# Optimization experiments

Hardware: AMD Instinct MI355X
Metric: run time of the kernel (lower is better)

## Reference

```python
import jax, jax.numpy as jnp
import numpy as np

FP8_MAX = 448.0  # torch.finfo(float8_e4m3fn).max


def per_tensor_quantize(t):
    amax = jnp.max(jnp.abs(t))
    scale = jnp.maximum(amax, 1e-12) / FP8_MAX
    q = jnp.clip(t / scale, -FP8_MAX, FP8_MAX)
    return q, scale.astype(jnp.float32)


def fp8_cast(t):
    # round-to-fp8-e4m3 and back (value-faithful to .to(float8_e4m3fn)),
    # straight-through so it is also usable under vjp
    rounded = t.astype(jnp.float8_e4m3fn).astype(t.dtype)
    return t + jax.lax.stop_gradient(rounded - t)


def setup_inputs() -> dict:
    key = jax.random.key(0)
    k1, k2, k3 = jax.random.split(key, 3)
    B, S, D_IN, D_OUT = 4, 2048, 4096, 4096
    x = jax.random.normal(k1, (B, S, D_IN), dtype=jnp.float32)
    # build a pre-quantized weight exactly like the repo would: quantize a float weight
    w = jax.random.normal(k2, (D_OUT, D_IN), dtype=jnp.float32) * 0.02
    qweight, weight_scale = per_tensor_quantize(w)
    bias = jax.random.normal(k3, (D_OUT,), dtype=jnp.float32) * 0.01
    return {"x": x, "qweight": qweight, "weight_scale": weight_scale, "bias": bias}


def reference(x, qweight, weight_scale, bias):
    quantize_output = True  # init kwarg
    # quantize activation per-tensor
    qinput, input_scale = per_tensor_quantize(x)
    qinput = fp8_cast(qinput)          # .to(float8_e4m3fn)
    qw = fp8_cast(qweight)             # .to(qdtype)
    # dequant-scaled GEMM: linear(A*sa, B*sb) + bias
    a = qinput * input_scale.astype(x.dtype)
    b = qw * weight_scale.astype(x.dtype)
    out = jnp.einsum('bsd,od->bso', a, b) + bias
    if quantize_output:
        qout, out_scale = per_tensor_quantize(out)  # clamp only, no fp8 cast (matches torch)
        out = qout * out_scale
    return out
```

## Files before the change

kernel.cpp:

```cpp
#include <hip/hip_runtime.h>
#include <stdint.h>

#define FP8_MAX 448.0f

typedef float f32x16 __attribute__((ext_vector_type(16)));
typedef int i32x8 __attribute__((ext_vector_type(8)));


__device__ __forceinline__ void async_load16(const void* gptr, void* lptr) {
  __builtin_amdgcn_global_load_lds(
      (const __attribute__((address_space(1))) unsigned int*)(uintptr_t)gptr,
      (__attribute__((address_space(3))) unsigned int*)(unsigned)(uintptr_t)lptr,
      16, 0, 0);
}

__device__ __forceinline__ unsigned pack4_fp8(float a, float b, float c, float d) {
  int v = __builtin_amdgcn_cvt_pk_fp8_f32(a, b, 0, false);
  v = __builtin_amdgcn_cvt_pk_fp8_f32(c, d, v, true);
  return (unsigned)v;
}

__device__ __forceinline__ float clip_fp8(float q) {
  return fminf(FP8_MAX, fmaxf(-FP8_MAX, q));
}

__device__ __forceinline__ i32x8 frag32(const unsigned char* rowbase, int o_lo) {
  uint4 lo = *(const uint4*)(rowbase + o_lo);
  uint4 hi = *(const uint4*)(rowbase + (o_lo ^ 16));
  i32x8 f;
  f[0] = lo.x; f[1] = lo.y; f[2] = lo.z; f[3] = lo.w;
  f[4] = hi.x; f[5] = hi.y; f[6] = hi.z; f[7] = hi.w;
  return f;
}


__global__ void k_amax(const float4* __restrict__ x, long n4, unsigned* __restrict__ out) {
  float m = 0.f;
  const long stride = (long)gridDim.x * blockDim.x;
  for (long i = (long)blockIdx.x * blockDim.x + threadIdx.x; i < n4; i += stride) {
    float4 v = x[i];
    m = fmaxf(m, fmaxf(fmaxf(fabsf(v.x), fabsf(v.y)), fmaxf(fabsf(v.z), fabsf(v.w))));
  }
#pragma unroll
  for (int off = 32; off > 0; off >>= 1)
    m = fmaxf(m, __shfl_xor(m, off, 64));
  __shared__ float sm[4];
  const int wv = threadIdx.x >> 6;
  if ((threadIdx.x & 63) == 0) sm[wv] = m;
  __syncthreads();
  if (threadIdx.x == 0) {
    m = fmaxf(fmaxf(sm[0], sm[1]), fmaxf(sm[2], sm[3]));
    atomicMax(out, __float_as_uint(m));
  }
}


__global__ void k_quant_x(const float4* __restrict__ x, unsigned* __restrict__ q,
                          const unsigned* __restrict__ amax_bits) {
  const float scale = fmaxf(__uint_as_float(*amax_bits), 1e-12f) / 448.0f;
  const long i0 = (long)blockIdx.x * blockDim.x + threadIdx.x;
  const long stride = (long)gridDim.x * blockDim.x;
#pragma unroll
  for (int r = 0; r < 4; r++) {
    const long i = i0 + r * stride;
    float4 v = x[i];
    q[i] = pack4_fp8(clip_fp8(v.x / scale), clip_fp8(v.y / scale),
                     clip_fp8(v.z / scale), clip_fp8(v.w / scale));
  }
}


__global__ void k_quant_w(const float4* __restrict__ w, unsigned* __restrict__ q) {
  const long i0 = (long)blockIdx.x * blockDim.x + threadIdx.x;
  const long stride = (long)gridDim.x * blockDim.x;
#pragma unroll
  for (int r = 0; r < 4; r++) {
    const long i = i0 + r * stride;
    float4 v = w[i];
    q[i] = pack4_fp8(clip_fp8(v.x), clip_fp8(v.y), clip_fp8(v.z), clip_fp8(v.w));
  }
}


__global__ __launch_bounds__(512, 2) void k_gemm(
    const unsigned char* __restrict__ qa, const unsigned char* __restrict__ qb,
    const unsigned* __restrict__ amax_bits, const float* __restrict__ wscale,
    const float* __restrict__ bias, float* __restrict__ out,
    int M, int N, int K) {
  __shared__ unsigned char lds[98304];

  const int t = threadIdx.x;
  const int lane = t & 63;
  const int wv = t >> 6;
  const int wm = wv >> 2;
  const int wn = wv & 3;
  const int lr = lane & 31;
  const int h = lane >> 5;
  const int key = (lr >> 1) & 3;

  const int bx = blockIdx.x;
  const int by = blockIdx.y;

  const unsigned char* Ag = qa + (size_t)by * 256 * K;
  const unsigned char* Bg = qb + (size_t)bx * 256 * K;

  size_t g_off[2]; int l_off[2];
#pragma unroll
  for (int r = 0; r < 2; r++) {
    const int idx = t + r * 512;
    const int row = idx >> 2;
    const int cs = idx & 3;
    g_off[r] = (size_t)row * K + (size_t)((cs ^ ((row >> 1) & 3)) << 4);
    l_off[r] = idx << 4;
  }

  const int o_lo = ((2 * h) ^ key) << 4;
  const int a_rowoff = (wm * 128 + lr) * 64;
  const int b_rowoff = (wn * 64 + lr) * 64;

  f32x16 acc[4][2];
#pragma unroll
  for (int i = 0; i < 4; i++)
#pragma unroll
    for (int j = 0; j < 2; j++)
#pragma unroll
      for (int r = 0; r < 16; r++) acc[i][j][r] = 0.f;

  int a0 = 0, a1 = 16384, a2 = 32768;
  int b0 = 49152, b1 = 65536, b2 = 81920;

#pragma unroll
  for (int r = 0; r < 2; r++) {
    async_load16(Ag + g_off[r], lds + a0 + l_off[r]);
    async_load16(Bg + g_off[r], lds + b0 + l_off[r]);
  }
#pragma unroll
  for (int r = 0; r < 2; r++) {
    async_load16(Ag + g_off[r] + 64, lds + a1 + l_off[r]);
    async_load16(Bg + g_off[r] + 64, lds + b1 + l_off[r]);
  }
  asm volatile("s_waitcnt vmcnt(4)" ::: "memory");
  __builtin_amdgcn_s_barrier();
  asm volatile("" ::: "memory");

  const int NT = K >> 6;
  for (int tile = 0; tile < NT; ++tile) {
    const bool haveS = (tile + 2 < NT);
    const size_t kb2 = (size_t)(tile + 2) << 6;
    const unsigned char* pa = lds + a0 + a_rowoff;
    const unsigned char* pb = lds + b0 + b_rowoff;

    i32x8 af0 = frag32(pa, o_lo);
    i32x8 af1 = frag32(pa + 2048, o_lo);
    i32x8 bf0 = frag32(pb, o_lo);
    i32x8 bf1 = frag32(pb + 2048, o_lo);
    if (haveS) {
#pragma unroll
      for (int r = 0; r < 2; r++)
        async_load16(Ag + g_off[r] + kb2, lds + a2 + l_off[r]);
#pragma unroll
      for (int r = 0; r < 2; r++)
        async_load16(Bg + g_off[r] + kb2, lds + b2 + l_off[r]);
    }
    i32x8 af2 = frag32(pa + 4096, o_lo);
    i32x8 af3 = frag32(pa + 6144, o_lo);

    __builtin_amdgcn_s_setprio(1);
    acc[0][0] = __builtin_amdgcn_mfma_scale_f32_32x32x64_f8f6f4(
        af0, bf0, acc[0][0], 0, 0, 0, 0x7f7f7f7f, 0, 0x7f7f7f7f);
    acc[0][1] = __builtin_amdgcn_mfma_scale_f32_32x32x64_f8f6f4(
        af0, bf1, acc[0][1], 0, 0, 0, 0x7f7f7f7f, 0, 0x7f7f7f7f);
    acc[1][0] = __builtin_amdgcn_mfma_scale_f32_32x32x64_f8f6f4(
        af1, bf0, acc[1][0], 0, 0, 0, 0x7f7f7f7f, 0, 0x7f7f7f7f);
    acc[1][1] = __builtin_amdgcn_mfma_scale_f32_32x32x64_f8f6f4(
        af1, bf1, acc[1][1], 0, 0, 0, 0x7f7f7f7f, 0, 0x7f7f7f7f);
    acc[2][0] = __builtin_amdgcn_mfma_scale_f32_32x32x64_f8f6f4(
        af2, bf0, acc[2][0], 0, 0, 0, 0x7f7f7f7f, 0, 0x7f7f7f7f);
    acc[2][1] = __builtin_amdgcn_mfma_scale_f32_32x32x64_f8f6f4(
        af2, bf1, acc[2][1], 0, 0, 0, 0x7f7f7f7f, 0, 0x7f7f7f7f);
    acc[3][0] = __builtin_amdgcn_mfma_scale_f32_32x32x64_f8f6f4(
        af3, bf0, acc[3][0], 0, 0, 0, 0x7f7f7f7f, 0, 0x7f7f7f7f);
    acc[3][1] = __builtin_amdgcn_mfma_scale_f32_32x32x64_f8f6f4(
        af3, bf1, acc[3][1], 0, 0, 0, 0x7f7f7f7f, 0, 0x7f7f7f7f);
    __builtin_amdgcn_s_setprio(0);

    if (haveS) {
      asm volatile("s_waitcnt vmcnt(4)" ::: "memory");
    } else {
      asm volatile("s_waitcnt vmcnt(0)" ::: "memory");
    }
    __builtin_amdgcn_s_barrier();
    asm volatile("" ::: "memory");

    int ta = a0; a0 = a1; a1 = a2; a2 = ta;
    int tb = b0; b0 = b1; b1 = b2; b2 = tb;
  }

  const float s_comb =
      (fmaxf(__uint_as_float(*amax_bits), 1e-12f) / 448.0f) * wscale[0];
#pragma unroll
  for (int nj = 0; nj < 2; ++nj) {
    const int col = bx * 256 + wn * 64 + nj * 32 + lr;
    const float bv = bias[col];
#pragma unroll
    for (int mi = 0; mi < 4; ++mi) {
      const int row0 = by * 256 + wm * 128 + mi * 32 + 4 * h;
#pragma unroll
      for (int r = 0; r < 16; ++r) {
        const int row = row0 + (r & 3) + 8 * (r >> 2);
        out[(size_t)row * N + col] = acc[mi][nj][r] * s_comb + bv;
      }
    }
  }
}


extern "C" void kernel_launch(void* const* d_in, const int* in_sizes, int n_in,
                              void* d_out, int out_size, void* d_ws, size_t ws_size,
                              hipStream_t stream) {
  const float* x = (const float*)d_in[0];
  const float* qw = (const float*)d_in[1];
  const float* wscale = (const float*)d_in[2];
  const float* bias = (const float*)d_in[3];

  const int N = in_sizes[3];
  const int K = in_sizes[1] / N;
  const int M = in_sizes[0] / K;

  const long nx = (long)M * K;
  const long nw = (long)N * K;

  unsigned char* ws = (unsigned char*)d_ws;
  unsigned* amax_bits = (unsigned*)ws;
  unsigned char* qx8 = ws + 256;
  unsigned char* qw8 = qx8 + nx;

  float* out = (float*)d_out;

  hipMemsetAsync(d_ws, 0, 4, stream);
  k_amax<<<2048, 256, 0, stream>>>((const float4*)x, nx / 4, amax_bits);
  k_quant_x<<<(int)(nx / 4 / 4 / 256), 256, 0, stream>>>(
      (const float4*)x, (unsigned*)qx8, amax_bits);
  k_quant_w<<<(int)(nw / 4 / 4 / 256), 256, 0, stream>>>(
      (const float4*)qw, (unsigned*)qw8);
  dim3 grid(N / 256, M / 256);
  k_gemm<<<grid, 512, 0, stream>>>(qx8, qw8, amax_bits, wscale, bias, out,
                                   M, N, K);
}
```

Measured before the change: 452.6 us.

## Software-pipeline LDS fragment loads with MFMAs via register double-buffering

The GEMM main loop is unrolled by two and now keeps two sets of B-fragment registers. The next tile's fragments are read from LDS while the current tile's second half of MFMAs is still issuing, instead of being read before any MFMA starts. The barrier and the global-to-LDS prefetch move to the middle of the tile body, and the wait becomes vmcnt(0). The intent is to hide LDS read latency behind matrix-core work, at the cost of more live registers and an unroll that assumes an even tile count.

```diff
diff --git a/kernel.cpp b/kernel.cpp
--- a/kernel.cpp
+++ b/kernel.cpp
@@ -82,6 +82,47 @@
 }
 
 
+#define MFMA_F8(d, a, b)                                                     \
+  d = __builtin_amdgcn_mfma_scale_f32_32x32x64_f8f6f4(a, b, d, 0, 0, 0,      \
+                                                      0x7f7f7f7f, 0, 0x7f7f7f7f)
+
+#define GEMM_BODY(T, bc0, bc1, bn0, bn1)                                     \
+  {                                                                          \
+    const bool hv1 = ((T) + 1 < NT);                                         \
+    const bool hv2 = ((T) + 2 < NT);                                         \
+    __builtin_amdgcn_s_setprio(1);                                           \
+    MFMA_F8(acc[0][0], af0, bc0); MFMA_F8(acc[0][1], af0, bc1);              \
+    MFMA_F8(acc[1][0], af1, bc0); MFMA_F8(acc[1][1], af1, bc1);              \
+    __builtin_amdgcn_s_setprio(0);                                           \
+    __builtin_amdgcn_sched_barrier(0);                                       \
+    if (hv1) {                                                               \
+      asm volatile("s_waitcnt vmcnt(0)" ::: "memory");                       \
+      __builtin_amdgcn_s_barrier();                                          \
+      const unsigned char* pa = lds + rA + a_rowoff;                         \
+      const unsigned char* pb = lds + rB + b_rowoff;                         \
+      af0 = frag32(pa, o_lo);                                                \
+      af1 = frag32(pa + 2048, o_lo);                                         \
+      bn0 = frag32(pb, o_lo);                                                \
+      bn1 = frag32(pb + 2048, o_lo);                                         \
+      if (hv2) {                                                             \
+        const size_t kb = (size_t)((T) + 2) << 6;                            \
+        async_load16(Ag + g_off[0] + kb, lds + sA + l_off[0]);               \
+        async_load16(Ag + g_off[1] + kb, lds + sA + l_off[1]);               \
+        async_load16(Bg + g_off[0] + kb, lds + sB + l_off[0]);               \
+        async_load16(Bg + g_off[1] + kb, lds + sB + l_off[1]);               \
+      }                                                                      \
+    }                                                                        \
+    __builtin_amdgcn_sched_barrier(0);                                       \
+    __builtin_amdgcn_s_setprio(1);                                           \
+    MFMA_F8(acc[2][0], af2, bc0); MFMA_F8(acc[2][1], af2, bc1);              \
+    if (hv1) af2 = frag32(lds + rA + a_rowoff + 4096, o_lo);                 \
+    MFMA_F8(acc[3][0], af3, bc0); MFMA_F8(acc[3][1], af3, bc1);              \
+    if (hv1) af3 = frag32(lds + rA + a_rowoff + 6144, o_lo);                 \
+    __builtin_amdgcn_s_setprio(0);                                           \
+    { int tmp = fA; fA = rA; rA = sA; sA = tmp; }                            \
+    { int tmp = fB; fB = rB; rB = sB; sB = tmp; }                            \
+  }
+
 __global__ __launch_bounds__(512, 2) void k_gemm(
     const unsigned char* __restrict__ qa, const unsigned char* __restrict__ qb,
     const unsigned* __restrict__ amax_bits, const float* __restrict__ wscale,
@@ -126,74 +167,38 @@
 #pragma unroll
       for (int r = 0; r < 16; r++) acc[i][j][r] = 0.f;
 
-  int a0 = 0, a1 = 16384, a2 = 32768;
-  int b0 = 49152, b1 = 65536, b2 = 81920;
+  int fA = 0, rA = 16384, sA = 32768;
+  int fB = 49152, rB = 65536, sB = 81920;
 
 #pragma unroll
   for (int r = 0; r < 2; r++) {
-    async_load16(Ag + g_off[r], lds + a0 + l_off[r]);
-    async_load16(Bg + g_off[r], lds + b0 + l_off[r]);
+    async_load16(Ag + g_off[r], lds + fA + l_off[r]);
+    async_load16(Bg + g_off[r], lds + fB + l_off[r]);
   }
 #pragma unroll
   for (int r = 0; r < 2; r++) {
-    async_load16(Ag + g_off[r] + 64, lds + a1 + l_off[r]);
-    async_load16(Bg + g_off[r] + 64, lds + b1 + l_off[r]);
+    async_load16(Ag + g_off[r] + 64, lds + rA + l_off[r]);
+    async_load16(Bg + g_off[r] + 64, lds + rB + l_off[r]);
   }
   asm volatile("s_waitcnt vmcnt(4)" ::: "memory");
   __builtin_amdgcn_s_barrier();
-  asm volatile("" ::: "memory");
+
+  i32x8 af0, af1, af2, af3, bfA0, bfA1, bfB0, bfB1;
+  {
+    const unsigned char* pa = lds + fA + a_rowoff;
+    const unsigned char* pb = lds + fB + b_rowoff;
+    af0 = frag32(pa, o_lo);
+    af1 = frag32(pa + 2048, o_lo);
+    af2 = frag32(pa + 4096, o_lo);
+    af3 = frag32(pa + 6144, o_lo);
+    bfA0 = frag32(pb, o_lo);
+    bfA1 = frag32(pb + 2048, o_lo);
+  }
 
   const int NT = K >> 6;
-  for (int tile = 0; tile < NT; ++tile) {
-    const bool haveS = (tile + 2 < NT);
-    const size_t kb2 = (size_t)(tile + 2) << 6;
-    const unsigned char* pa = lds + a0 + a_rowoff;
-    const unsigned char* pb = lds + b0 + b_rowoff;
-
-    i32x8 af0 = frag32(pa, o_lo);
-    i32x8 af1 = frag32(pa + 2048, o_lo);
-    i32x8 bf0 = frag32(pb, o_lo);
-    i32x8 bf1 = frag32(pb + 2048, o_lo);
-    if (haveS) {
-#pragma unroll
-      for (int r = 0; r < 2; r++)
-        async_load16(Ag + g_off[r] + kb2, lds + a2 + l_off[r]);
-#pragma unroll
-      for (int r = 0; r < 2; r++)
-        async_load16(Bg + g_off[r] + kb2, lds + b2 + l_off[r]);
-    }
-    i32x8 af2 = frag32(pa + 4096, o_lo);
-    i32x8 af3 = frag32(pa + 6144, o_lo);
-
-    __builtin_amdgcn_s_setprio(1);
-    acc[0][0] = __builtin_amdgcn_mfma_scale_f32_32x32x64_f8f6f4(
-        af0, bf0, acc[0][0], 0, 0, 0, 0x7f7f7f7f, 0, 0x7f7f7f7f);
-    acc[0][1] = __builtin_amdgcn_mfma_scale_f32_32x32x64_f8f6f4(
-        af0, bf1, acc[0][1], 0, 0, 0, 0x7f7f7f7f, 0, 0x7f7f7f7f);
-    acc[1][0] = __builtin_amdgcn_mfma_scale_f32_32x32x64_f8f6f4(
-        af1, bf0, acc[1][0], 0, 0, 0, 0x7f7f7f7f, 0, 0x7f7f7f7f);
-    acc[1][1] = __builtin_amdgcn_mfma_scale_f32_32x32x64_f8f6f4(
-        af1, bf1, acc[1][1], 0, 0, 0, 0x7f7f7f7f, 0, 0x7f7f7f7f);
-    acc[2][0] = __builtin_amdgcn_mfma_scale_f32_32x32x64_f8f6f4(
-        af2, bf0, acc[2][0], 0, 0, 0, 0x7f7f7f7f, 0, 0x7f7f7f7f);
-    acc[2][1] = __builtin_amdgcn_mfma_scale_f32_32x32x64_f8f6f4(
-        af2, bf1, acc[2][1], 0, 0, 0, 0x7f7f7f7f, 0, 0x7f7f7f7f);
-    acc[3][0] = __builtin_amdgcn_mfma_scale_f32_32x32x64_f8f6f4(
-        af3, bf0, acc[3][0], 0, 0, 0, 0x7f7f7f7f, 0, 0x7f7f7f7f);
-    acc[3][1] = __builtin_amdgcn_mfma_scale_f32_32x32x64_f8f6f4(
-        af3, bf1, acc[3][1], 0, 0, 0, 0x7f7f7f7f, 0, 0x7f7f7f7f);
-    __builtin_amdgcn_s_setprio(0);
-
-    if (haveS) {
-      asm volatile("s_waitcnt vmcnt(4)" ::: "memory");
-    } else {
-      asm volatile("s_waitcnt vmcnt(0)" ::: "memory");
-    }
-    __builtin_amdgcn_s_barrier();
-    asm volatile("" ::: "memory");
-
-    int ta = a0; a0 = a1; a1 = a2; a2 = ta;
-    int tb = b0; b0 = b1; b1 = b2; b2 = tb;
+  for (int tt = 0; tt < NT; tt += 2) {
+    GEMM_BODY(tt, bfA0, bfA1, bfB0, bfB1);
+    GEMM_BODY(tt + 1, bfB0, bfB1, bfA0, bfA1);
   }
 
   const float s_comb =
```

Result: slower. 893.8 us (+97.5%).
